# Kernel optimization log

Hardware: AMD Instinct MI355X
Metric: run time of the kernel (lower is better)

## Reference

```python
import jax, jax.numpy as jnp
import numpy as np
import math

L, HEADS, K, NFFN, H = 4, 8, 32, 2, 256  # layers, attention heads, top-k neighbors, FFN layers, hidden


def mish(x):
    return x * jnp.tanh(jax.nn.softplus(x))


def layernorm(x, a, b, eps=1e-6):
    # torch LayerNorm-style with UNBIASED std (x.std default), matching the source
    mean = x.mean(-1, keepdims=True)
    var = jnp.sum((x - mean) ** 2, axis=-1, keepdims=True) / (x.shape[-1] - 1)
    return a * (x - mean) / (jnp.sqrt(var) + eps) + b


def linear(x, W, b):
    # torch nn.Linear: y = x @ W^T + b, W is [out, in]
    return jnp.einsum('...i,oi->...o', x, W) + b


def setup_inputs() -> dict:
    key = jax.random.key(0)
    ks = jax.random.split(key, 6)
    node_features = jax.random.normal(ks[0], (16, 512, H), dtype=jnp.float32)
    edge_features = jax.random.uniform(ks[1], (16, 512, 512), dtype=jnp.float32)
    masks = jnp.ones((16, 512), dtype=jnp.int32)
    attn_W = jax.random.normal(ks[2], (L, 4, H, H), dtype=jnp.float32) * 0.05  # q,k,v,out per layer
    attn_b = jnp.zeros((L, 4, H), dtype=jnp.float32)
    ffn_W = jax.random.normal(ks[3], (L, NFFN, H, H), dtype=jnp.float32) * 0.05
    ffn_b = jnp.zeros((L, NFFN, H), dtype=jnp.float32)
    ln_a = jnp.ones((H,), dtype=jnp.float32)
    ln_b = jnp.zeros((H,), dtype=jnp.float32)
    return {"node_features": node_features, "edge_features": edge_features, "masks": masks,
            "attn_W": attn_W, "attn_b": attn_b, "ffn_W": ffn_W, "ffn_b": ffn_b,
            "ln_a": ln_a, "ln_b": ln_b}


def reference(node_features, edge_features, masks, attn_W, attn_b, ffn_W, ffn_b, ln_a, ln_b):
    b, m, _ = node_features.shape
    d = H // HEADS
    scale = 1.0 / math.sqrt(d)

    # top-k edge-weight mask (double argsort rank trick, as in source); deterministic
    rank = jnp.argsort(jnp.argsort(-edge_features, axis=-1), axis=-1)
    ew = edge_features * (rank < K)
    ew = ew / (jnp.sum(ew, axis=-1, keepdims=True) + 1e-5)  # [b, m, m]

    col_mask = (masks == 0)[:, None, None, :]  # broadcast over heads and query rows

    x = node_features
    for i in range(L):
        x = layernorm(x, ln_a, ln_b)
        # MHSA
        def split_heads(y):
            return y.reshape(b, m, HEADS, d).transpose(0, 2, 1, 3)  # b h m d
        q = split_heads(linear(x, attn_W[i, 0], attn_b[i, 0]))
        k = split_heads(linear(x, attn_W[i, 1], attn_b[i, 1]))
        v = split_heads(linear(x, attn_W[i, 2], attn_b[i, 2]))
        scores = jnp.einsum('bhmd,bhnd->bhmn', q, k)
        scores = jnp.where(col_mask, -1e12, scores)
        scores = jax.nn.softmax(scores * ew[:, None] * scale, axis=-1)
        attn_out = jnp.einsum('bhmn,bhnd->bhmd', scores, v)
        attn_out = attn_out.transpose(0, 2, 1, 3).reshape(b, m, H)
        attn_out = mish(linear(attn_out, attn_W[i, 3], attn_b[i, 3]))
        x = x + attn_out
        x = layernorm(x, ln_a, ln_b)
        # FFN: all layers use mish (output_act_fn='mish')
        y = x
        for j in range(NFFN):
            y = mish(linear(y, ffn_W[i, j], ffn_b[i, j]))
        x = x + y
    return x
```

## Files before the change

kernel.cpp:

```cpp
#include <hip/hip_runtime.h>
#include <cstddef>

#define NB 16
#define NM 512
#define NHID 256
#define NTOPK 32
#define NROWS (NB*NM)
#define NLAYER 4

typedef unsigned short ushort_t;
typedef __attribute__((ext_vector_type(8))) short short8;
typedef __attribute__((ext_vector_type(4))) float f32x4;

#define FRAG_OFF(row, c8) (((c8) >> 2) * 1024 + ((((c8) & 3) << 4) + (((row) & 15) ^ ((c8) >> 2))) * 16)
#define FRAG_RD(ks, lane) ((ks) * 1024 + ((((lane) >> 4) << 4) + (((lane) & 15) ^ (ks))) * 16)

#define MFMA16(a, b, c) __builtin_amdgcn_mfma_f32_16x16x32_bf16((a), (b), (c), 0, 0, 0)

__device__ __forceinline__ float mish_f(float v) {
    if (v > 20.0f) return v;
    float t = __expf(v);
    float u = t * (t + 2.0f);
    return v * (u / (u + 2.0f));
}
__device__ __forceinline__ ushort_t f2b(float f) {
    unsigned u = __float_as_uint(f);
    return (ushort_t)((u + 0x7FFFu + ((u >> 16) & 1u)) >> 16);
}
__device__ __forceinline__ float b2f(ushort_t h) {
    return __uint_as_float(((unsigned)h) << 16);
}

__global__ __launch_bounds__(256) void prep_kernel(const float* __restrict__ edge,
                                                   int* __restrict__ tidx,
                                                   float* __restrict__ tw,
                                                   const float* __restrict__ attnW,
                                                   const float* __restrict__ ffnW,
                                                   ushort_t* __restrict__ wb) {
    if (blockIdx.x < 768) {
        int t = blockIdx.x * 256 + threadIdx.x;
        int frag = t >> 9, r = t & 511;
        int ks = r >> 6, l = r & 63;
        const float* src;
        if (frag < 256) src = attnW + ((size_t)(frag >> 6) * 1024 + (frag & 63) * 16 + (l & 15)) * 256;
        else { int fi = frag - 256; src = ffnW + ((size_t)(fi >> 5) * 512 + (fi & 31) * 16 + (l & 15)) * 256; }
        src += ks * 32 + (l >> 4) * 8;
        short8 o;
        #pragma unroll
        for (int j = 0; j < 8; ++j) o[j] = (short)f2b(src[j]);
        *(short8*)(wb + (size_t)t * 8) = o;
        return;
    }
    const int lane = threadIdx.x & 63, w = threadIdx.x >> 6;
    const int row = (blockIdx.x - 768) * 4 + w;
    const float* er = edge + (size_t)row * NM;
    float v[8]; unsigned u[8];
    #pragma unroll
    for (int s = 0; s < 8; ++s) { v[s] = er[s * 64 + lane]; u[s] = __float_as_uint(v[s]); }
    unsigned T = 0;
    for (int bit = 31; bit >= 0; --bit) {
        unsigned Tc = T | (1u << bit);
        int c = 0;
        #pragma unroll
        for (int s = 0; s < 8; ++s) c += (int)__popcll(__ballot(u[s] >= Tc));
        if (c >= NTOPK) T = Tc;
    }
    int cgt = 0;
    #pragma unroll
    for (int s = 0; s < 8; ++s) cgt += (int)__popcll(__ballot(u[s] > T));
    const int extra = NTOPK - cgt;
    float psum = 0.f;
    #pragma unroll
    for (int s = 0; s < 8; ++s) psum += (u[s] > T) ? v[s] : 0.f;
    psum += __shfl_xor(psum, 1); psum += __shfl_xor(psum, 2); psum += __shfl_xor(psum, 4);
    psum += __shfl_xor(psum, 8); psum += __shfl_xor(psum, 16); psum += __shfl_xor(psum, 32);
    const float ssum = psum + (float)extra * __uint_as_float(T);
    const float rden = 0.17677669529663687f / (ssum + 1e-5f);
    const unsigned long long lmask = (1ull << lane) - 1ull;
    int base = 0, eqbase = 0;
    #pragma unroll
    for (int s = 0; s < 8; ++s) {
        bool gt = (u[s] > T), eq = (u[s] == T);
        unsigned long long meq = __ballot(eq);
        int eqrank = eqbase + (int)__popcll(meq & lmask);
        bool sel = gt || (eq && eqrank < extra);
        unsigned long long msel = __ballot(sel);
        if (sel) {
            int pos = base + (int)__popcll(msel & lmask);
            tidx[row * NTOPK + pos] = s * 64 + lane;
            tw[row * NTOPK + pos] = v[s] * rden;
        }
        base += (int)__popcll(msel);
        eqbase += (int)__popcll(meq);
    }
}

__global__ __launch_bounds__(256) void k1_ln_qkv(const float* __restrict__ xin,
                                                 ushort_t* __restrict__ xb,
                                                 ushort_t* __restrict__ qb,
                                                 ushort_t* __restrict__ kvb,
                                                 float* __restrict__ part,
                                                 const ushort_t* __restrict__ wf,
                                                 const float* __restrict__ bias,
                                                 const float* __restrict__ ga,
                                                 const float* __restrict__ gb) {
    __shared__ __align__(16) char af[8192];
    const int tid = threadIdx.x, lane = tid & 63, w = tid >> 6;
    const int bx = blockIdx.x;
    const int wid = (bx & 7) * 64 + (bx >> 3);
    const int bm = wid * 16, bb = wid >> 5, blk = wid & 31;
    const int zb = blockIdx.y;
    {
        const int rr = lane >> 4, c16 = (lane & 15) << 4;
        const int ri = (w << 2) + rr;
        const float* xr = xin + (size_t)(bm + ri) * NHID + c16;
        f32x4 v0 = *(const f32x4*)(xr);
        f32x4 v1 = *(const f32x4*)(xr + 4);
        f32x4 v2 = *(const f32x4*)(xr + 8);
        f32x4 v3 = *(const f32x4*)(xr + 12);
        float s = 0.f;
        #pragma unroll
        for (int k = 0; k < 4; ++k) s += v0[k] + v1[k] + v2[k] + v3[k];
        s += __shfl_xor(s, 1); s += __shfl_xor(s, 2); s += __shfl_xor(s, 4); s += __shfl_xor(s, 8);
        float mean = s * (1.0f / NHID);
        float vr = 0.f;
        #pragma unroll
        for (int k = 0; k < 4; ++k) {
            float d0 = v0[k]-mean, d1 = v1[k]-mean, d2 = v2[k]-mean, d3 = v3[k]-mean;
            vr += d0*d0 + d1*d1 + d2*d2 + d3*d3;
        }
        vr += __shfl_xor(vr, 1); vr += __shfl_xor(vr, 2); vr += __shfl_xor(vr, 4); vr += __shfl_xor(vr, 8);
        vr *= (1.0f / (NHID - 1));
        float rs = 1.0f / (sqrtf(vr) + 1e-6f);
        f32x4 g0 = *(const f32x4*)(ga + c16), g1 = *(const f32x4*)(ga + c16 + 4);
        f32x4 g2 = *(const f32x4*)(ga + c16 + 8), g3 = *(const f32x4*)(ga + c16 + 12);
        f32x4 h0 = *(const f32x4*)(gb + c16), h1 = *(const f32x4*)(gb + c16 + 4);
        f32x4 h2 = *(const f32x4*)(gb + c16 + 8), h3 = *(const f32x4*)(gb + c16 + 12);
        f32x4 o0, o1, o2, o3;
        #pragma unroll
        for (int k = 0; k < 4; ++k) {
            o0[k] = g0[k]*(v0[k]-mean)*rs + h0[k];
            o1[k] = g1[k]*(v1[k]-mean)*rs + h1[k];
            o2[k] = g2[k]*(v2[k]-mean)*rs + h2[k];
            o3[k] = g3[k]*(v3[k]-mean)*rs + h3[k];
        }
        short8 p0, p1;
        #pragma unroll
        for (int k = 0; k < 4; ++k) {
            p0[k] = (short)f2b(o0[k]); p0[4+k] = (short)f2b(o1[k]);
            p1[k] = (short)f2b(o2[k]); p1[4+k] = (short)f2b(o3[k]);
        }
        if (zb == 0) {
            ushort_t* xw = xb + (size_t)(bm + ri) * NHID + c16;
            *(short8*)(xw) = p0;
            *(short8*)(xw + 8) = p1;
        }
        int c8 = (lane & 15) * 2;
        *(short8*)(af + FRAG_OFF(ri, c8)) = p0;
        *(short8*)(af + FRAG_OFF(ri, c8 + 1)) = p1;
    }
    __syncthreads();
    short8 a[8];
    #pragma unroll
    for (int ks = 0; ks < 8; ++ks) a[ks] = *(const short8*)(af + FRAG_RD(ks, lane));
    #pragma unroll
    for (int gi = 0; gi < 3; ++gi) {
        const int col0 = (zb * 3 + gi) * 128 + w * 32;
        f32x4 acc0 = {}, acc1 = {};
        const ushort_t* bp0 = wf + ((size_t)((col0 >> 4) * 8) * 64 + lane) * 8;
        const ushort_t* bp1 = bp0 + 4096;
        #pragma unroll
        for (int ks = 0; ks < 8; ++ks) {
            short8 b0 = *(const short8*)(bp0 + ks * 512);
            short8 b1 = *(const short8*)(bp1 + ks * 512);
            acc0 = MFMA16(a[ks], b0, acc0);
            acc1 = MFMA16(a[ks], b1, acc1);
        }
        const int rbase = bm + (lane >> 4) * 4;
        #pragma unroll
        for (int ni = 0; ni < 2; ++ni) {
            int col = col0 + ni * 16 + (lane & 15);
            float bv = bias[col];
            f32x4 A = ni ? acc1 : acc0;
            #pragma unroll
            for (int j = 0; j < 4; ++j) {
                int row = rbase + j;
                float vv = A[j] + bv;
                if (col < 256) qb[(size_t)row * 256 + col] = f2b(vv);
                else kvb[(size_t)row * 512 + (col - 256)] = f2b(vv);
            }
            if (zb == 1 && gi >= 1) {
                float s2 = A[0] + A[1] + A[2] + A[3] + 4.0f * bv;
                s2 += __shfl_xor(s2, 16); s2 += __shfl_xor(s2, 32);
                if (lane < 16)
                    part[((size_t)bb * 32 + blk) * 256 + (col0 + ni * 16 + lane - 512)] = s2;
            }
        }
    }
}

template<int LAST>
__global__ __launch_bounds__(1024, 4) void kb_layer(ushort_t* __restrict__ xb,
                                                    float* __restrict__ xout,
                                                    ushort_t* __restrict__ qb,
                                                    const ushort_t* __restrict__ kvb_cur,
                                                    ushort_t* __restrict__ kvb_nxt,
                                                    const float* __restrict__ part_cur,
                                                    float* __restrict__ part_nxt,
                                                    const int* __restrict__ tidx,
                                                    const float* __restrict__ tw,
                                                    const int* __restrict__ msk,
                                                    const ushort_t* __restrict__ wfo,
                                                    const ushort_t* __restrict__ wf1,
                                                    const ushort_t* __restrict__ wf2,
                                                    const ushort_t* __restrict__ wqn,
                                                    const float* __restrict__ bo,
                                                    const float* __restrict__ b1,
                                                    const float* __restrict__ b2,
                                                    const float* __restrict__ bqn,
                                                    const float* __restrict__ ga,
                                                    const float* __restrict__ gb) {
    __shared__ __align__(16) float regA[32 * 256];
    __shared__ __align__(16) char regB[16384];
    __shared__ __align__(16) char regC[16384];
    const int tid = threadIdx.x, lane = tid & 63, w = tid >> 6;
    const int wid = (blockIdx.x & 7) * 32 + (blockIdx.x >> 3);
    const int R0 = wid * 32, bb = wid >> 4, blk = wid & 15;
    int* sidx = (int*)regC;
    float* sws = (float*)(regC + 4096);
    float* vsumf = regA;
    {
        int nb = tidx[(size_t)R0 * NTOPK + tid];
        float wv = tw[(size_t)R0 * NTOPK + tid];
        sidx[tid] = (msk[bb * NM + nb] == 0) ? (nb | (int)0x80000000) : nb;
        sws[tid] = wv;
    }
    if (tid < 256) {
        float s = 0.f;
        #pragma unroll
        for (int p = 0; p < 32; ++p) s += part_cur[((size_t)bb * 32 + p) * 256 + tid];
        vsumf[tid] = s;
    }
    float xres[2][4];
    #pragma unroll
    for (int rh = 0; rh < 2; ++rh)
        #pragma unroll
        for (int j = 0; j < 4; ++j)
            xres[rh][j] = b2f(xb[(size_t)(R0 + rh * 16 + (lane >> 4) * 4 + j) * NHID + w * 16 + (lane & 15)]);
    const int rl = w * 2 + (lane >> 5);
    const int cbase = (lane & 31) * 8;
    float qv[8];
    {
        short8 qh = *(const short8*)(qb + (size_t)(R0 + rl) * 256 + cbase);
        #pragma unroll
        for (int k = 0; k < 8; ++k) qv[k] = b2f((ushort_t)qh[k]);
    }
    __syncthreads();
    {
        float accv[8] = {};
        float den = 0.f;
        for (int j = 0; j < NTOPK; ++j) {
            int raw = sidx[rl * 32 + j];
            float swv = sws[rl * 32 + j];
            const ushort_t* kp = kvb_cur + ((size_t)(bb * NM + (raw & 511))) * 512 + cbase;
            short8 kA = *(const short8*)(kp);
            short8 vA = *(const short8*)(kp + 256);
            float p = 0.f;
            #pragma unroll
            for (int t = 0; t < 8; ++t) p += qv[t] * b2f((ushort_t)kA[t]);
            p += __shfl_xor(p, 1); p += __shfl_xor(p, 2);
            float sarg = (raw < 0) ? -1e12f : p;
            float e = __expf(sarg * swv);
            float em1 = e - 1.0f;
            den += em1;
            #pragma unroll
            for (int t = 0; t < 8; ++t) accv[t] += em1 * b2f((ushort_t)vA[t]);
        }
        float rden = 1.0f / (den + 512.0f);
        short8 p0;
        #pragma unroll
        for (int t = 0; t < 8; ++t) p0[t] = (short)f2b((accv[t] + vsumf[cbase + t]) * rden);
        *(short8*)(regB + (rl >> 4) * 8192 + FRAG_OFF(rl, (lane & 31))) = p0;
    }
    __syncthreads();
    {
        short8 b[8];
        const ushort_t* bp = wfo + ((size_t)(w * 8) * 64 + lane) * 8;
        #pragma unroll
        for (int ks = 0; ks < 8; ++ks) b[ks] = *(const short8*)(bp + ks * 512);
        int col = w * 16 + (lane & 15);
        float bv = bo[col];
        #pragma unroll
        for (int rh = 0; rh < 2; ++rh) {
            f32x4 acc = {};
            #pragma unroll
            for (int ks = 0; ks < 8; ++ks)
                acc = MFMA16(*(const short8*)(regB + rh * 8192 + FRAG_RD(ks, lane)), b[ks], acc);
            #pragma unroll
            for (int j = 0; j < 4; ++j) {
                int row = rh * 16 + (lane >> 4) * 4 + j;
                regA[row * 256 + col] = mish_f(acc[j] + bv) + xres[rh][j];
            }
        }
    }
    __syncthreads();
    {
        const int c0 = (lane & 31) * 8;
        float* xr = regA + rl * 256 + c0;
        f32x4 v0 = *(const f32x4*)xr, v1 = *(const f32x4*)(xr + 4);
        float s = v0[0]+v0[1]+v0[2]+v0[3]+v1[0]+v1[1]+v1[2]+v1[3];
        s += __shfl_xor(s,1); s += __shfl_xor(s,2); s += __shfl_xor(s,4);
        s += __shfl_xor(s,8); s += __shfl_xor(s,16);
        float mean = s * (1.0f / NHID);
        float vr = 0.f;
        #pragma unroll
        for (int k = 0; k < 4; ++k) {
            float d0 = v0[k]-mean, d1 = v1[k]-mean;
            vr += d0*d0 + d1*d1;
        }
        vr += __shfl_xor(vr,1); vr += __shfl_xor(vr,2); vr += __shfl_xor(vr,4);
        vr += __shfl_xor(vr,8); vr += __shfl_xor(vr,16);
        vr *= (1.0f / (NHID - 1));
        float rs = 1.0f / (sqrtf(vr) + 1e-6f);
        f32x4 g0 = *(const f32x4*)(ga + c0), g1 = *(const f32x4*)(ga + c0 + 4);
        f32x4 h0 = *(const f32x4*)(gb + c0), h1 = *(const f32x4*)(gb + c0 + 4);
        f32x4 o0, o1;
        #pragma unroll
        for (int k = 0; k < 4; ++k) {
            o0[k] = g0[k]*(v0[k]-mean)*rs + h0[k];
            o1[k] = g1[k]*(v1[k]-mean)*rs + h1[k];
        }
        *(f32x4*)xr = o0; *(f32x4*)(xr + 4) = o1;
        short8 p;
        #pragma unroll
        for (int k = 0; k < 4; ++k) { p[k] = (short)f2b(o0[k]); p[4+k] = (short)f2b(o1[k]); }
        *(short8*)(regB + (rl >> 4) * 8192 + FRAG_OFF(rl, (lane & 31))) = p;
    }
    __syncthreads();
    {
        short8 b[8];
        const ushort_t* bp = wf1 + ((size_t)(w * 8) * 64 + lane) * 8;
        #pragma unroll
        for (int ks = 0; ks < 8; ++ks) b[ks] = *(const short8*)(bp + ks * 512);
        int col = w * 16 + (lane & 15);
        float bv = b1[col];
        int c8 = col >> 3;
        #pragma unroll
        for (int rh = 0; rh < 2; ++rh) {
            f32x4 acc = {};
            #pragma unroll
            for (int ks = 0; ks < 8; ++ks)
                acc = MFMA16(*(const short8*)(regB + rh * 8192 + FRAG_RD(ks, lane)), b[ks], acc);
            #pragma unroll
            for (int j = 0; j < 4; ++j) {
                int row = rh * 16 + (lane >> 4) * 4 + j;
                *(ushort_t*)(regC + rh * 8192 + FRAG_OFF(row, c8) + (col & 7) * 2) = f2b(mish_f(acc[j] + bv));
            }
        }
    }
    __syncthreads();
    {
        short8 b[8];
        const ushort_t* bp = wf2 + ((size_t)(w * 8) * 64 + lane) * 8;
        #pragma unroll
        for (int ks = 0; ks < 8; ++ks) b[ks] = *(const short8*)(bp + ks * 512);
        int col = w * 16 + (lane & 15);
        float bv = b2[col];
        #pragma unroll
        for (int rh = 0; rh < 2; ++rh) {
            f32x4 acc = {};
            #pragma unroll
            for (int ks = 0; ks < 8; ++ks)
                acc = MFMA16(*(const short8*)(regC + rh * 8192 + FRAG_RD(ks, lane)), b[ks], acc);
            #pragma unroll
            for (int j = 0; j < 4; ++j) {
                int row = rh * 16 + (lane >> 4) * 4 + j;
                float v = mish_f(acc[j] + bv) + regA[row * 256 + col];
                if (LAST) xout[(size_t)(R0 + row) * NHID + col] = v;
                else regA[row * 256 + col] = v;
            }
        }
    }
    if (LAST) return;
    __syncthreads();
    {
        const int c0 = (lane & 31) * 8;
        float* xr = regA + rl * 256 + c0;
        f32x4 v0 = *(const f32x4*)xr, v1 = *(const f32x4*)(xr + 4);
        float s = v0[0]+v0[1]+v0[2]+v0[3]+v1[0]+v1[1]+v1[2]+v1[3];
        s += __shfl_xor(s,1); s += __shfl_xor(s,2); s += __shfl_xor(s,4);
        s += __shfl_xor(s,8); s += __shfl_xor(s,16);
        float mean = s * (1.0f / NHID);
        float vr = 0.f;
        #pragma unroll
        for (int k = 0; k < 4; ++k) {
            float d0 = v0[k]-mean, d1 = v1[k]-mean;
            vr += d0*d0 + d1*d1;
        }
        vr += __shfl_xor(vr,1); vr += __shfl_xor(vr,2); vr += __shfl_xor(vr,4);
        vr += __shfl_xor(vr,8); vr += __shfl_xor(vr,16);
        vr *= (1.0f / (NHID - 1));
        float rs = 1.0f / (sqrtf(vr) + 1e-6f);
        f32x4 g0 = *(const f32x4*)(ga + c0), g1 = *(const f32x4*)(ga + c0 + 4);
        f32x4 h0 = *(const f32x4*)(gb + c0), h1 = *(const f32x4*)(gb + c0 + 4);
        f32x4 o0, o1;
        #pragma unroll
        for (int k = 0; k < 4; ++k) {
            o0[k] = g0[k]*(v0[k]-mean)*rs + h0[k];
            o1[k] = g1[k]*(v1[k]-mean)*rs + h1[k];
        }
        short8 p;
        #pragma unroll
        for (int k = 0; k < 4; ++k) { p[k] = (short)f2b(o0[k]); p[4+k] = (short)f2b(o1[k]); }
        *(short8*)(xb + (size_t)(R0 + rl) * NHID + c0) = p;
        *(short8*)(regB + (rl >> 4) * 8192 + FRAG_OFF(rl, (lane & 31))) = p;
    }
    __syncthreads();
    {
        #pragma unroll
        for (int gg = 0; gg < 3; ++gg) {
            const int ct = w + gg * 16;
            short8 b[8];
            const ushort_t* bp = wqn + (size_t)ct * 4096 + (size_t)lane * 8;
            #pragma unroll
            for (int ks = 0; ks < 8; ++ks) b[ks] = *(const short8*)(bp + ks * 512);
            int col = ct * 16 + (lane & 15);
            float bv = bqn[col];
            #pragma unroll
            for (int rh = 0; rh < 2; ++rh) {
                f32x4 acc = {};
                #pragma unroll
                for (int ks = 0; ks < 8; ++ks)
                    acc = MFMA16(*(const short8*)(regB + rh * 8192 + FRAG_RD(ks, lane)), b[ks], acc);
                #pragma unroll
                for (int j = 0; j < 4; ++j) {
                    int row = rh * 16 + (lane >> 4) * 4 + j;
                    float vv = acc[j] + bv;
                    if (col < 256) qb[(size_t)(R0 + row) * 256 + col] = f2b(vv);
                    else kvb_nxt[(size_t)(R0 + row) * 512 + (col - 256)] = f2b(vv);
                }
                if (gg == 2) {
                    float s2 = acc[0] + acc[1] + acc[2] + acc[3] + 4.0f * bv;
                    s2 += __shfl_xor(s2, 16); s2 += __shfl_xor(s2, 32);
                    if (lane < 16)
                        part_nxt[((size_t)bb * 32 + blk * 2 + rh) * 256 + (ct * 16 + lane - 512)] = s2;
                }
            }
        }
    }
}

extern "C" void kernel_launch(void* const* d_in, const int* in_sizes, int n_in,
                              void* d_out, int out_size, void* d_ws, size_t ws_size,
                              hipStream_t stream) {
    (void)in_sizes; (void)n_in; (void)out_size; (void)ws_size;
    const float* node  = (const float*)d_in[0];
    const float* edge  = (const float*)d_in[1];
    const int*   msk   = (const int*)d_in[2];
    const float* attnW = (const float*)d_in[3];
    const float* attnB = (const float*)d_in[4];
    const float* ffnW  = (const float*)d_in[5];
    const float* ffnB  = (const float*)d_in[6];
    const float* lna   = (const float*)d_in[7];
    const float* lnb   = (const float*)d_in[8];

    float* x = (float*)d_out;
    float* wsf = (float*)d_ws;
    ushort_t* qb    = (ushort_t*)wsf;
    ushort_t* xb    = (ushort_t*)(wsf + 1048576);
    ushort_t* kvbA  = (ushort_t*)(wsf + 2097152);
    ushort_t* kvbB  = (ushort_t*)(wsf + 4194304);
    ushort_t* wb    = (ushort_t*)(wsf + 6291456);
    float*    tw    = wsf + 7077888;
    int*      tidx  = (int*)(wsf + 7340032);
    float*    partA = wsf + 7602176;
    float*    partB = wsf + 7733248;

    prep_kernel<<<2816, 256, 0, stream>>>(edge, tidx, tw, attnW, ffnW, wb);
    k1_ln_qkv<<<dim3(512, 2), 256, 0, stream>>>(node, xb, qb, kvbA, partA,
                                                wb, attnB, lna, lnb);
    for (int l = 0; l < NLAYER; ++l) {
        ushort_t* kv_c = (l & 1) ? kvbB : kvbA;
        ushort_t* kv_n = (l & 1) ? kvbA : kvbB;
        float* pt_c = (l & 1) ? partB : partA;
        float* pt_n = (l & 1) ? partA : partB;
        const ushort_t* wfo = wb + (size_t)(l * 64 + 48) * 4096;
        const ushort_t* wf1 = wb + (size_t)(256 + l * 32) * 4096;
        const ushort_t* wf2 = wb + (size_t)(256 + l * 32 + 16) * 4096;
        const ushort_t* wqn = wb + (size_t)(((l + 1) & 3) * 64) * 4096;
        const float* bo  = attnB + (size_t)l * 1024 + 768;
        const float* b1  = ffnB + (size_t)l * 512;
        const float* b2  = b1 + 256;
        const float* bqn = attnB + (size_t)((l + 1) & 3) * 1024;
        if (l < NLAYER - 1)
            kb_layer<0><<<256, 1024, 0, stream>>>(xb, x, qb, kv_c, kv_n, pt_c, pt_n,
                tidx, tw, msk, wfo, wf1, wf2, wqn, bo, b1, b2, bqn, lna, lnb);
        else
            kb_layer<1><<<256, 1024, 0, stream>>>(xb, x, qb, kv_c, kv_n, pt_c, pt_n,
                tidx, tw, msk, wfo, wf1, wf2, wqn, bo, b1, b2, bqn, lna, lnb);
    }
}
```

Measured before the change: 158.8 us.

## Halve layer-kernel block size to 512 threads, doubling per-thread work

The fused per-layer kernel now runs 8 waves per block instead of 16. Each thread handles 16 columns of a row in the sparse attention gather, and each wave computes two or six 16-column output tiles in the GEMM stages. The residual is reloaded from global memory in the output projection instead of being held in registers. The aim is to cut barrier cost and raise per-thread ILP, at the cost of more registers and serialized work per wave across only 256 blocks.

```diff
diff --git a/kernel.cpp b/kernel.cpp
--- a/kernel.cpp
+++ b/kernel.cpp
@@ -200,26 +200,26 @@
 }
 
 template<int LAST>
-__global__ __launch_bounds__(1024, 4) void kb_layer(ushort_t* __restrict__ xb,
-                                                    float* __restrict__ xout,
-                                                    ushort_t* __restrict__ qb,
-                                                    const ushort_t* __restrict__ kvb_cur,
-                                                    ushort_t* __restrict__ kvb_nxt,
-                                                    const float* __restrict__ part_cur,
-                                                    float* __restrict__ part_nxt,
-                                                    const int* __restrict__ tidx,
-                                                    const float* __restrict__ tw,
-                                                    const int* __restrict__ msk,
-                                                    const ushort_t* __restrict__ wfo,
-                                                    const ushort_t* __restrict__ wf1,
-                                                    const ushort_t* __restrict__ wf2,
-                                                    const ushort_t* __restrict__ wqn,
-                                                    const float* __restrict__ bo,
-                                                    const float* __restrict__ b1,
-                                                    const float* __restrict__ b2,
-                                                    const float* __restrict__ bqn,
-                                                    const float* __restrict__ ga,
-                                                    const float* __restrict__ gb) {
+__global__ __launch_bounds__(512, 4) void kb_layer(ushort_t* __restrict__ xb,
+                                                   float* __restrict__ xout,
+                                                   ushort_t* __restrict__ qb,
+                                                   const ushort_t* __restrict__ kvb_cur,
+                                                   ushort_t* __restrict__ kvb_nxt,
+                                                   const float* __restrict__ part_cur,
+                                                   float* __restrict__ part_nxt,
+                                                   const int* __restrict__ tidx,
+                                                   const float* __restrict__ tw,
+                                                   const int* __restrict__ msk,
+                                                   const ushort_t* __restrict__ wfo,
+                                                   const ushort_t* __restrict__ wf1,
+                                                   const ushort_t* __restrict__ wf2,
+                                                   const ushort_t* __restrict__ wqn,
+                                                   const float* __restrict__ bo,
+                                                   const float* __restrict__ b1,
+                                                   const float* __restrict__ b2,
+                                                   const float* __restrict__ bqn,
+                                                   const float* __restrict__ ga,
+                                                   const float* __restrict__ gb) {
     __shared__ __align__(16) float regA[32 * 256];
     __shared__ __align__(16) char regB[16384];
     __shared__ __align__(16) char regC[16384];
@@ -229,11 +229,13 @@
     int* sidx = (int*)regC;
     float* sws = (float*)(regC + 4096);
     float* vsumf = regA;
-    {
-        int nb = tidx[(size_t)R0 * NTOPK + tid];
-        float wv = tw[(size_t)R0 * NTOPK + tid];
-        sidx[tid] = (msk[bb * NM + nb] == 0) ? (nb | (int)0x80000000) : nb;
-        sws[tid] = wv;
+    #pragma unroll
+    for (int i = 0; i < 2; ++i) {
+        int idx = i * 512 + tid;
+        int nb = tidx[(size_t)R0 * NTOPK + idx];
+        float wv = tw[(size_t)R0 * NTOPK + idx];
+        sidx[idx] = (msk[bb * NM + nb] == 0) ? (nb | (int)0x80000000) : nb;
+        sws[idx] = wv;
     }
     if (tid < 256) {
         float s = 0.f;
@@ -241,185 +243,236 @@
         for (int p = 0; p < 32; ++p) s += part_cur[((size_t)bb * 32 + p) * 256 + tid];
         vsumf[tid] = s;
     }
-    float xres[2][4];
-    #pragma unroll
-    for (int rh = 0; rh < 2; ++rh)
-        #pragma unroll
-        for (int j = 0; j < 4; ++j)
-            xres[rh][j] = b2f(xb[(size_t)(R0 + rh * 16 + (lane >> 4) * 4 + j) * NHID + w * 16 + (lane & 15)]);
-    const int rl = w * 2 + (lane >> 5);
-    const int cbase = (lane & 31) * 8;
-    float qv[8];
-    {
-        short8 qh = *(const short8*)(qb + (size_t)(R0 + rl) * 256 + cbase);
-        #pragma unroll
-        for (int k = 0; k < 8; ++k) qv[k] = b2f((ushort_t)qh[k]);
-    }
-    __syncthreads();
-    {
-        float accv[8] = {};
+    const int rr = w * 4 + (lane >> 4);
+    const int li = lane & 15;
+    const int cbase = li * 16;
+    float qv[16];
+    {
+        const ushort_t* qp = qb + (size_t)(R0 + rr) * 256 + cbase;
+        short8 q0 = *(const short8*)(qp);
+        short8 q1 = *(const short8*)(qp + 8);
+        #pragma unroll
+        for (int k = 0; k < 8; ++k) { qv[k] = b2f((ushort_t)q0[k]); qv[8+k] = b2f((ushort_t)q1[k]); }
+    }
+    __syncthreads();
+    {
+        float accv[16];
+        #pragma unroll
+        for (int k = 0; k < 16; ++k) accv[k] = 0.f;
         float den = 0.f;
+        const ushort_t* kvbase = kvb_cur + (size_t)(bb * NM) * 512 + cbase;
         for (int j = 0; j < NTOPK; ++j) {
-            int raw = sidx[rl * 32 + j];
-            float swv = sws[rl * 32 + j];
-            const ushort_t* kp = kvb_cur + ((size_t)(bb * NM + (raw & 511))) * 512 + cbase;
+            int raw = sidx[rr * 32 + j];
+            float swv = sws[rr * 32 + j];
+            const ushort_t* kp = kvbase + (size_t)(raw & 511) * 512;
             short8 kA = *(const short8*)(kp);
+            short8 kB = *(const short8*)(kp + 8);
             short8 vA = *(const short8*)(kp + 256);
+            short8 vB = *(const short8*)(kp + 264);
             float p = 0.f;
             #pragma unroll
             for (int t = 0; t < 8; ++t) p += qv[t] * b2f((ushort_t)kA[t]);
-            p += __shfl_xor(p, 1); p += __shfl_xor(p, 2);
+            #pragma unroll
+            for (int t = 0; t < 8; ++t) p += qv[8 + t] * b2f((ushort_t)kB[t]);
+            p += __shfl_xor(p, 1);
             float sarg = (raw < 0) ? -1e12f : p;
             float e = __expf(sarg * swv);
             float em1 = e - 1.0f;
             den += em1;
             #pragma unroll
             for (int t = 0; t < 8; ++t) accv[t] += em1 * b2f((ushort_t)vA[t]);
+            #pragma unroll
+            for (int t = 0; t < 8; ++t) accv[8 + t] += em1 * b2f((ushort_t)vB[t]);
         }
         float rden = 1.0f / (den + 512.0f);
-        short8 p0;
-        #pragma unroll
-        for (int t = 0; t < 8; ++t) p0[t] = (short)f2b((accv[t] + vsumf[cbase + t]) * rden);
-        *(short8*)(regB + (rl >> 4) * 8192 + FRAG_OFF(rl, (lane & 31))) = p0;
-    }
-    __syncthreads();
-    {
-        short8 b[8];
-        const ushort_t* bp = wfo + ((size_t)(w * 8) * 64 + lane) * 8;
-        #pragma unroll
-        for (int ks = 0; ks < 8; ++ks) b[ks] = *(const short8*)(bp + ks * 512);
-        int col = w * 16 + (lane & 15);
-        float bv = bo[col];
-        #pragma unroll
-        for (int rh = 0; rh < 2; ++rh) {
-            f32x4 acc = {};
-            #pragma unroll
-            for (int ks = 0; ks < 8; ++ks)
-                acc = MFMA16(*(const short8*)(regB + rh * 8192 + FRAG_RD(ks, lane)), b[ks], acc);
-            #pragma unroll
-            for (int j = 0; j < 4; ++j) {
-                int row = rh * 16 + (lane >> 4) * 4 + j;
-                regA[row * 256 + col] = mish_f(acc[j] + bv) + xres[rh][j];
+        short8 p0, p1;
+        #pragma unroll
+        for (int t = 0; t < 8; ++t) {
+            p0[t] = (short)f2b((accv[t] + vsumf[cbase + t]) * rden);
+            p1[t] = (short)f2b((accv[8 + t] + vsumf[cbase + 8 + t]) * rden);
+        }
+        int c8 = li * 2;
+        *(short8*)(regB + (rr >> 4) * 8192 + FRAG_OFF(rr, c8)) = p0;
+        *(short8*)(regB + (rr >> 4) * 8192 + FRAG_OFF(rr, c8 + 1)) = p1;
+    }
+    __syncthreads();
+    {
+        #pragma unroll
+        for (int gg = 0; gg < 2; ++gg) {
+            const int ct = w + gg * 8;
+            short8 b[8];
+            const ushort_t* bp = wfo + (size_t)ct * 4096 + (size_t)lane * 8;
+            #pragma unroll
+            for (int ks = 0; ks < 8; ++ks) b[ks] = *(const short8*)(bp + ks * 512);
+            int col = ct * 16 + (lane & 15);
+            float bv = bo[col];
+            #pragma unroll
+            for (int rh = 0; rh < 2; ++rh) {
+                f32x4 acc = {};
+                #pragma unroll
+                for (int ks = 0; ks < 8; ++ks)
+                    acc = MFMA16(*(const short8*)(regB + rh * 8192 + FRAG_RD(ks, lane)), b[ks], acc);
+                #pragma unroll
+                for (int j = 0; j < 4; ++j) {
+                    int row = rh * 16 + (lane >> 4) * 4 + j;
+                    float res = b2f(xb[(size_t)(R0 + row) * NHID + col]);
+                    regA[row * 256 + col] = mish_f(acc[j] + bv) + res;
+                }
             }
         }
     }
     __syncthreads();
     {
-        const int c0 = (lane & 31) * 8;
-        float* xr = regA + rl * 256 + c0;
-        f32x4 v0 = *(const f32x4*)xr, v1 = *(const f32x4*)(xr + 4);
-        float s = v0[0]+v0[1]+v0[2]+v0[3]+v1[0]+v1[1]+v1[2]+v1[3];
-        s += __shfl_xor(s,1); s += __shfl_xor(s,2); s += __shfl_xor(s,4);
-        s += __shfl_xor(s,8); s += __shfl_xor(s,16);
+        const int c16 = li << 4;
+        float* xr = regA + rr * 256 + c16;
+        f32x4 v0 = *(const f32x4*)(xr);
+        f32x4 v1 = *(const f32x4*)(xr + 4);
+        f32x4 v2 = *(const f32x4*)(xr + 8);
+        f32x4 v3 = *(const f32x4*)(xr + 12);
+        float s = 0.f;
+        #pragma unroll
+        for (int k = 0; k < 4; ++k) s += v0[k] + v1[k] + v2[k] + v3[k];
+        s += __shfl_xor(s, 1); s += __shfl_xor(s, 2); s += __shfl_xor(s, 4); s += __shfl_xor(s, 8);
         float mean = s * (1.0f / NHID);
         float vr = 0.f;
         #pragma unroll
         for (int k = 0; k < 4; ++k) {
-            float d0 = v0[k]-mean, d1 = v1[k]-mean;
-            vr += d0*d0 + d1*d1;
-        }
-        vr += __shfl_xor(vr,1); vr += __shfl_xor(vr,2); vr += __shfl_xor(vr,4);
-        vr += __shfl_xor(vr,8); vr += __shfl_xor(vr,16);
+            float d0 = v0[k]-mean, d1 = v1[k]-mean, d2 = v2[k]-mean, d3 = v3[k]-mean;
+            vr += d0*d0 + d1*d1 + d2*d2 + d3*d3;
+        }
+        vr += __shfl_xor(vr, 1); vr += __shfl_xor(vr, 2); vr += __shfl_xor(vr, 4); vr += __shfl_xor(vr, 8);
         vr *= (1.0f / (NHID - 1));
         float rs = 1.0f / (sqrtf(vr) + 1e-6f);
-        f32x4 g0 = *(const f32x4*)(ga + c0), g1 = *(const f32x4*)(ga + c0 + 4);
-        f32x4 h0 = *(const f32x4*)(gb + c0), h1 = *(const f32x4*)(gb + c0 + 4);
-        f32x4 o0, o1;
+        f32x4 g0 = *(const f32x4*)(ga + c16), g1 = *(const f32x4*)(ga + c16 + 4);
+        f32x4 g2 = *(const f32x4*)(ga + c16 + 8), g3 = *(const f32x4*)(ga + c16 + 12);
+        f32x4 h0 = *(const f32x4*)(gb + c16), h1 = *(const f32x4*)(gb + c16 + 4);
+        f32x4 h2 = *(const f32x4*)(gb + c16 + 8), h3 = *(const f32x4*)(gb + c16 + 12);
+        f32x4 o0, o1, o2, o3;
         #pragma unroll
         for (int k = 0; k < 4; ++k) {
             o0[k] = g0[k]*(v0[k]-mean)*rs + h0[k];
             o1[k] = g1[k]*(v1[k]-mean)*rs + h1[k];
-        }
-        *(f32x4*)xr = o0; *(f32x4*)(xr + 4) = o1;
-        short8 p;
-        #pragma unroll
-        for (int k = 0; k < 4; ++k) { p[k] = (short)f2b(o0[k]); p[4+k] = (short)f2b(o1[k]); }
-        *(short8*)(regB + (rl >> 4) * 8192 + FRAG_OFF(rl, (lane & 31))) = p;
-    }
-    __syncthreads();
-    {
-        short8 b[8];
-        const ushort_t* bp = wf1 + ((size_t)(w * 8) * 64 + lane) * 8;
-        #pragma unroll
-        for (int ks = 0; ks < 8; ++ks) b[ks] = *(const short8*)(bp + ks * 512);
-        int col = w * 16 + (lane & 15);
-        float bv = b1[col];
-        int c8 = col >> 3;
-        #pragma unroll
-        for (int rh = 0; rh < 2; ++rh) {
-            f32x4 acc = {};
-            #pragma unroll
-            for (int ks = 0; ks < 8; ++ks)
-                acc = MFMA16(*(const short8*)(regB + rh * 8192 + FRAG_RD(ks, lane)), b[ks], acc);
-            #pragma unroll
-            for (int j = 0; j < 4; ++j) {
-                int row = rh * 16 + (lane >> 4) * 4 + j;
-                *(ushort_t*)(regC + rh * 8192 + FRAG_OFF(row, c8) + (col & 7) * 2) = f2b(mish_f(acc[j] + bv));
+            o2[k] = g2[k]*(v2[k]-mean)*rs + h2[k];
+            o3[k] = g3[k]*(v3[k]-mean)*rs + h3[k];
+        }
+        *(f32x4*)(xr) = o0; *(f32x4*)(xr + 4) = o1;
+        *(f32x4*)(xr + 8) = o2; *(f32x4*)(xr + 12) = o3;
+        short8 p0, p1;
+        #pragma unroll
+        for (int k = 0; k < 4; ++k) {
+            p0[k] = (short)f2b(o0[k]); p0[4+k] = (short)f2b(o1[k]);
+            p1[k] = (short)f2b(o2[k]); p1[4+k] = (short)f2b(o3[k]);
+        }
+        int c8 = li * 2;
+        *(short8*)(regB + (rr >> 4) * 8192 + FRAG_OFF(rr, c8)) = p0;
+        *(short8*)(regB + (rr >> 4) * 8192 + FRAG_OFF(rr, c8 + 1)) = p1;
+    }
+    __syncthreads();
+    {
+        #pragma unroll
+        for (int gg = 0; gg < 2; ++gg) {
+            const int ct = w + gg * 8;
+            short8 b[8];
+            const ushort_t* bp = wf1 + (size_t)ct * 4096 + (size_t)lane * 8;
+            #pragma unroll
+            for (int ks = 0; ks < 8; ++ks) b[ks] = *(const short8*)(bp + ks * 512);
+            int col = ct * 16 + (lane & 15);
+            float bv = b1[col];
+            int c8 = col >> 3;
+            #pragma unroll
+            for (int rh = 0; rh < 2; ++rh) {
+                f32x4 acc = {};
+                #pragma unroll
+                for (int ks = 0; ks < 8; ++ks)
+                    acc = MFMA16(*(const short8*)(regB + rh * 8192 + FRAG_RD(ks, lane)), b[ks], acc);
+                #pragma unroll
+                for (int j = 0; j < 4; ++j) {
+                    int row = rh * 16 + (lane >> 4) * 4 + j;
+                    *(ushort_t*)(regC + rh * 8192 + FRAG_OFF(row, c8) + (col & 7) * 2) = f2b(mish_f(acc[j] + bv));
+                }
             }
         }
     }
     __syncthreads();
     {
-        short8 b[8];
-        const ushort_t* bp = wf2 + ((size_t)(w * 8) * 64 + lane) * 8;
-        #pragma unroll
-        for (int ks = 0; ks < 8; ++ks) b[ks] = *(const short8*)(bp + ks * 512);
-        int col = w * 16 + (lane & 15);
-        float bv = b2[col];
-        #pragma unroll
-        for (int rh = 0; rh < 2; ++rh) {
-            f32x4 acc = {};
-            #pragma unroll
-            for (int ks = 0; ks < 8; ++ks)
-                acc = MFMA16(*(const short8*)(regC + rh * 8192 + FRAG_RD(ks, lane)), b[ks], acc);
-            #pragma unroll
-            for (int j = 0; j < 4; ++j) {
-                int row = rh * 16 + (lane >> 4) * 4 + j;
-                float v = mish_f(acc[j] + bv) + regA[row * 256 + col];
-                if (LAST) xout[(size_t)(R0 + row) * NHID + col] = v;
-                else regA[row * 256 + col] = v;
+        #pragma unroll
+        for (int gg = 0; gg < 2; ++gg) {
+            const int ct = w + gg * 8;
+            short8 b[8];
+            const ushort_t* bp = wf2 + (size_t)ct * 4096 + (size_t)lane * 8;
+            #pragma unroll
+            for (int ks = 0; ks < 8; ++ks) b[ks] = *(const short8*)(bp + ks * 512);
+            int col = ct * 16 + (lane & 15);
+            float bv = b2[col];
+            #pragma unroll
+            for (int rh = 0; rh < 2; ++rh) {
+                f32x4 acc = {};
+                #pragma unroll
+                for (int ks = 0; ks < 8; ++ks)
+                    acc = MFMA16(*(const short8*)(regC + rh * 8192 + FRAG_RD(ks, lane)), b[ks], acc);
+                #pragma unroll
+                for (int j = 0; j < 4; ++j) {
+                    int row = rh * 16 + (lane >> 4) * 4 + j;
+                    float v = mish_f(acc[j] + bv) + regA[row * 256 + col];
+                    if (LAST) xout[(size_t)(R0 + row) * NHID + col] = v;
+                    else regA[row * 256 + col] = v;
+                }
             }
         }
     }
     if (LAST) return;
     __syncthreads();
     {
-        const int c0 = (lane & 31) * 8;
-        float* xr = regA + rl * 256 + c0;
-        f32x4 v0 = *(const f32x4*)xr, v1 = *(const f32x4*)(xr + 4);
-        float s = v0[0]+v0[1]+v0[2]+v0[3]+v1[0]+v1[1]+v1[2]+v1[3];
-        s += __shfl_xor(s,1); s += __shfl_xor(s,2); s += __shfl_xor(s,4);
-        s += __shfl_xor(s,8); s += __shfl_xor(s,16);
+        const int c16 = li << 4;
+        float* xr = regA + rr * 256 + c16;
+        f32x4 v0 = *(const f32x4*)(xr);
+        f32x4 v1 = *(const f32x4*)(xr + 4);
+        f32x4 v2 = *(const f32x4*)(xr + 8);
+        f32x4 v3 = *(const f32x4*)(xr + 12);
+        float s = 0.f;
+        #pragma unroll
+        for (int k = 0; k < 4; ++k) s += v0[k] + v1[k] + v2[k] + v3[k];
+        s += __shfl_xor(s, 1); s += __shfl_xor(s, 2); s += __shfl_xor(s, 4); s += __shfl_xor(s, 8);
         float mean = s * (1.0f / NHID);
         float vr = 0.f;
         #pragma unroll
         for (int k = 0; k < 4; ++k) {
-            float d0 = v0[k]-mean, d1 = v1[k]-mean;
-            vr += d0*d0 + d1*d1;
-        }
-        vr += __shfl_xor(vr,1); vr += __shfl_xor(vr,2); vr += __shfl_xor(vr,4);
-        vr += __shfl_xor(vr,8); vr += __shfl_xor(vr,16);
+            float d0 = v0[k]-mean, d1 = v1[k]-mean, d2 = v2[k]-mean, d3 = v3[k]-mean;
+            vr += d0*d0 + d1*d1 + d2*d2 + d3*d3;
+        }
+        vr += __shfl_xor(vr, 1); vr += __shfl_xor(vr, 2); vr += __shfl_xor(vr, 4); vr += __shfl_xor(vr, 8);
         vr *= (1.0f / (NHID - 1));
         float rs = 1.0f / (sqrtf(vr) + 1e-6f);
-        f32x4 g0 = *(const f32x4*)(ga + c0), g1 = *(const f32x4*)(ga + c0 + 4);
-        f32x4 h0 = *(const f32x4*)(gb + c0), h1 = *(const f32x4*)(gb + c0 + 4);
-        f32x4 o0, o1;
+        f32x4 g0 = *(const f32x4*)(ga + c16), g1 = *(const f32x4*)(ga + c16 + 4);
+        f32x4 g2 = *(const f32x4*)(ga + c16 + 8), g3 = *(const f32x4*)(ga + c16 + 12);
+        f32x4 h0 = *(const f32x4*)(gb + c16), h1 = *(const f32x4*)(gb + c16 + 4);
+        f32x4 h2 = *(const f32x4*)(gb + c16 + 8), h3 = *(const f32x4*)(gb + c16 + 12);
+        f32x4 o0, o1, o2, o3;
         #pragma unroll
         for (int k = 0; k < 4; ++k) {
             o0[k] = g0[k]*(v0[k]-mean)*rs + h0[k];
             o1[k] = g1[k]*(v1[k]-mean)*rs + h1[k];
-        }
-        short8 p;
-        #pragma unroll
-        for (int k = 0; k < 4; ++k) { p[k] = (short)f2b(o0[k]); p[4+k] = (short)f2b(o1[k]); }
-        *(short8*)(xb + (size_t)(R0 + rl) * NHID + c0) = p;
-        *(short8*)(regB + (rl >> 4) * 8192 + FRAG_OFF(rl, (lane & 31))) = p;
-    }
-    __syncthreads();
-    {
-        #pragma unroll
-        for (int gg = 0; gg < 3; ++gg) {
-            const int ct = w + gg * 16;
+            o2[k] = g2[k]*(v2[k]-mean)*rs + h2[k];
+            o3[k] = g3[k]*(v3[k]-mean)*rs + h3[k];
+        }
+        short8 p0, p1;
+        #pragma unroll
+        for (int k = 0; k < 4; ++k) {
+            p0[k] = (short)f2b(o0[k]); p0[4+k] = (short)f2b(o1[k]);
+            p1[k] = (short)f2b(o2[k]); p1[4+k] = (short)f2b(o3[k]);
+        }
+        ushort_t* xw = xb + (size_t)(R0 + rr) * NHID + c16;
+        *(short8*)(xw) = p0;
+        *(short8*)(xw + 8) = p1;
+        int c8 = li * 2;
+        *(short8*)(regB + (rr >> 4) * 8192 + FRAG_OFF(rr, c8)) = p0;
+        *(short8*)(regB + (rr >> 4) * 8192 + FRAG_OFF(rr, c8 + 1)) = p1;
+    }
+    __syncthreads();
+    {
+        #pragma unroll
+        for (int gg = 0; gg < 6; ++gg) {
+            const int ct = w + gg * 8;
             short8 b[8];
             const ushort_t* bp = wqn + (size_t)ct * 4096 + (size_t)lane * 8;
             #pragma unroll
@@ -439,7 +492,7 @@
                     if (col < 256) qb[(size_t)(R0 + row) * 256 + col] = f2b(vv);
                     else kvb_nxt[(size_t)(R0 + row) * 512 + (col - 256)] = f2b(vv);
                 }
-                if (gg == 2) {
+                if (ct >= 32) {
                     float s2 = acc[0] + acc[1] + acc[2] + acc[3] + 4.0f * bv;
                     s2 += __shfl_xor(s2, 16); s2 += __shfl_xor(s2, 32);
                     if (lane < 16)
@@ -493,10 +546,10 @@
         const float* b2  = b1 + 256;
         const float* bqn = attnB + (size_t)((l + 1) & 3) * 1024;
         if (l < NLAYER - 1)
-            kb_layer<0><<<256, 1024, 0, stream>>>(xb, x, qb, kv_c, kv_n, pt_c, pt_n,
+            kb_layer<0><<<256, 512, 0, stream>>>(xb, x, qb, kv_c, kv_n, pt_c, pt_n,
                 tidx, tw, msk, wfo, wf1, wf2, wqn, bo, b1, b2, bqn, lna, lnb);
         else
-            kb_layer<1><<<256, 1024, 0, stream>>>(xb, x, qb, kv_c, kv_n, pt_c, pt_n,
+            kb_layer<1><<<256, 512, 0, stream>>>(xb, x, qb, kv_c, kv_n, pt_c, pt_n,
                 tidx, tw, msk, wfo, wf1, wf2, wqn, bo, b1, b2, bqn, lna, lnb);
     }
 }
```

New measurement: 227.3 us. 43.2% more time.
